# Optimization experiments

Measured on AMD Instinct MI355X. Metric: run time of the kernel, lower is better.

## Reference

```python
import jax, jax.numpy as jnp
import numpy as np

SAMPLE_RATE = 48000.0
WIN_SIZE = 512   # also the FFT size (nfft = win_size in forward)
HOP_SIZE = 256   # win_size // 2, COLA with Hann
B = 128
NUM_FREQ_PTS = 96000  # 2 s RIR at 48 kHz


def _hann(n):
    # torch.hann_window default is periodic: 0.5*(1 - cos(2*pi*k/n))
    k = jnp.arange(n, dtype=jnp.float32)
    return 0.5 * (1.0 - jnp.cos(2.0 * jnp.pi * k / n))


def _stft(x, win, nfft, hop):
    # x: [B, L] real. center=False, onesided=True, not normalized.
    L = x.shape[-1]
    pad = (-L) % hop  # pad to multiple of hop, as in get_stft_torch
    if pad:
        x = jnp.pad(x, ((0, 0), (0, pad)))
    T = (x.shape[-1] - nfft) // hop + 1  # number of frames
    idx = hop * jnp.arange(T)[:, None] + jnp.arange(nfft)[None, :]  # [T, nfft]
    frames = x[:, idx] * win  # [B, T, nfft]
    return jnp.fft.rfft(frames, n=nfft, axis=-1)  # [B, T, F], F = nfft//2 + 1


def _edr_db(S):
    # S: [B, T, F] complex. EDR[m] = sum_{t>=m} |S[t]|^2  -> reverse cumsum (O(T)).
    P = jnp.abs(S) ** 2  # [B, T, F]
    edr = jnp.flip(jnp.cumsum(jnp.flip(P, axis=1), axis=1), axis=1)
    return 10.0 * jnp.log10(edr)  # db(..., is_squared=True)


def reference(target_re, target_im, ach_re, ach_im):
    n = target_re.shape[-1]
    target_rir = jnp.fft.irfft(target_re + 1j * target_im, n=n)
    ach_rir = jnp.fft.irfft(ach_re + 1j * ach_im, n=n)
    win = _hann(WIN_SIZE)
    S_t = _stft(target_rir, win, WIN_SIZE, HOP_SIZE)
    S_a = _stft(ach_rir, win, WIN_SIZE, HOP_SIZE)
    edr_t = _edr_db(S_t)
    edr_a = _edr_db(S_a)
    return jnp.sum(jnp.abs(edr_t - edr_a)) / jnp.sum(jnp.abs(edr_t))


def setup_inputs() -> dict:
    key = jax.random.key(0)
    k1, k2, k3, k4 = jax.random.split(key, 4)
    shape = (B, NUM_FREQ_PTS)
    return {
        "target_re": jax.random.normal(k1, shape, dtype=jnp.float32),
        "target_im": jax.random.normal(k2, shape, dtype=jnp.float32),
        "ach_re": jax.random.normal(k3, shape, dtype=jnp.float32),
        "ach_im": jax.random.normal(k4, shape, dtype=jnp.float32),
    }
```

## Files before the change

### kernel.cpp

```cpp
#include <hip/hip_runtime.h>
#include <math.h>

#define BATCH   128
#define NFREQ   96000
#define M_HALF  48000
#define NFRAMES 374
#define NBINS   257
#define NG      11
#define GLEN    34
#define FPW     4

#define PI_D 3.14159265358979323846

__device__ __forceinline__ float2 cmulf(float2 a, float2 b) {
  return make_float2(a.x * b.x - a.y * b.y, a.x * b.y + a.y * b.x);
}

__device__ __forceinline__ void bfly4(float2 z0, float2 z1, float2 z2, float2 z3,
                                      float2& o0, float2& o1, float2& o2, float2& o3) {
  float2 e0 = make_float2(z0.x + z2.x, z0.y + z2.y);
  float2 e1 = make_float2(z0.x - z2.x, z0.y - z2.y);
  float2 e2 = make_float2(z1.x + z3.x, z1.y + z3.y);
  float2 e3 = make_float2(z1.x - z3.x, z1.y - z3.y);
  o0 = make_float2(e0.x + e2.x, e0.y + e2.y);
  o2 = make_float2(e0.x - e2.x, e0.y - e2.y);
  o1 = make_float2(e1.x + e3.y, e1.y - e3.x);
  o3 = make_float2(e1.x - e3.y, e1.y + e3.x);
}

#define PIDX(i) ((i) + ((i) >> 3))

__global__ void setup_kernel(float2* __restrict__ Wm, float2* __restrict__ Wpack,
                             float2* __restrict__ W512, float* __restrict__ hann) {
  int i = blockIdx.x * blockDim.x + threadIdx.x;
  if (i < M_HALF) {
    double th = 2.0 * PI_D * (double)i / (double)M_HALF;
    double s, c; sincos(th, &s, &c);
    Wm[i] = make_float2((float)c, (float)s);
    double th2 = PI_D * (double)i / (double)M_HALF;
    double s2, c2; sincos(th2, &s2, &c2);
    Wpack[i] = make_float2((float)c2, (float)s2);
  }
  if (i < 512) {
    double th = -2.0 * PI_D * (double)i / 512.0;
    double s, c; sincos(th, &s, &c);
    W512[i] = make_float2((float)c, (float)s);
    hann[i] = (float)(0.5 * (1.0 - cos(2.0 * PI_D * (double)i / 512.0)));
  }
}

__global__ __launch_bounds__(256) void pack_kernel(
    const float* __restrict__ tre, const float* __restrict__ tim,
    const float* __restrict__ are, const float* __restrict__ aim,
    float2* __restrict__ A, const float2* __restrict__ Wpack, int b0, int c) {
  int idx = blockIdx.x * blockDim.x + threadIdx.x;
  int total = 2 * c * M_HALF;
  if (idx >= total) return;
  int row = idx / M_HALF;
  int k = idx - row * M_HALF;
  int isA = row >= c;
  int b = b0 + (isA ? row - c : row);
  const float* re = isA ? are : tre;
  const float* im = isA ? aim : tim;
  const float* rr = re + (size_t)b * NFREQ;
  const float* ii = im + (size_t)b * NFREQ;
  float xr = rr[k];
  float xi = (k == 0) ? 0.f : ii[k];
  int mk = M_HALF - k;
  float yr = rr[mk];
  float yi = (mk == M_HALF) ? 0.f : ii[mk];
  float Er = 0.5f * (xr + yr);
  float Ei = 0.5f * (xi - yi);
  float Dr = 0.5f * (xr - yr);
  float Di = 0.5f * (xi + yi);
  float2 wp = Wpack[k];
  float tr = wp.x * Dr - wp.y * Di;
  float ti = wp.x * Di + wp.y * Dr;
  const float sc = 1.0f / (float)M_HALF;
  A[(size_t)row * M_HALF + k] = make_float2((Er - ti) * sc, (Ei + tr) * sc);
}

template <int R, int S, int NN>
__global__ __launch_bounds__(256) void stage_kernel(
    const float2* __restrict__ x, float2* __restrict__ y,
    const float2* __restrict__ Wm, int rows) {
  constexpr int MM = NN / R;
  constexpr int ITEMS = M_HALF / R;
  int idx = blockIdx.x * blockDim.x + threadIdx.x;
  if (idx >= rows * ITEMS) return;
  int row = idx / ITEMS;
  int t = idx - row * ITEMS;
  int q = t % S;
  int p = t / S;
  const float2* xr = x + (size_t)row * M_HALF;
  float2* yr = y + (size_t)row * M_HALF;
  float2 a[R];
#pragma unroll
  for (int j = 0; j < R; ++j) a[j] = xr[q + S * (p + MM * j)];
  float2 wr[R];
#pragma unroll
  for (int t2 = 0; t2 < R; ++t2) wr[t2] = Wm[t2 * (M_HALF / R)];
  float2 twb = Wm[(size_t)p * (M_HALF / NN)];
  float2 tw = make_float2(1.f, 0.f);
#pragma unroll
  for (int u = 0; u < R; ++u) {
    float2 acc = a[0];
#pragma unroll
    for (int j = 1; j < R; ++j) {
      float2 w = wr[(u * j) % R];
      acc.x += a[j].x * w.x - a[j].y * w.y;
      acc.y += a[j].x * w.y + a[j].y * w.x;
    }
    acc = cmulf(acc, tw);
    yr[q + S * (R * p + u)] = acc;
    tw = cmulf(tw, twb);
  }
}

__global__ __launch_bounds__(256) void stft256_kernel(
    const float* __restrict__ xtime, float* __restrict__ P,
    const float2* __restrict__ W512, const float* __restrict__ hann) {
  __shared__ float2 lds[4][2][288];
  const int tid = threadIdx.x;
  const int wave = tid >> 6;
  const int l = tid & 63;
  const int row = blockIdx.y;
  const int frame0 = (blockIdx.x * 4 + wave) * FPW;

  float2* Abuf = lds[wave][0];
  float2* Bbuf = lds[wave][1];

  const float2* hann2 = (const float2*)hann;
  float2 hw[4];
#pragma unroll
  for (int j = 0; j < 4; ++j) hw[j] = hann2[l + 64 * j];
  float2 t1[3], t2[3], t3[3];
  {
    int p2 = l >> 2, p3 = l >> 4;
#pragma unroll
    for (int u = 1; u <= 3; ++u) {
      t1[u - 1] = W512[2 * u * l];
      t2[u - 1] = W512[8 * u * p2];
      t3[u - 1] = W512[32 * u * p3];
    }
  }

  const float2* xrow = (const float2*)xtime + (size_t)row * 48000;

  for (int fi = 0; fi < FPW; ++fi) {
    const int fr = frame0 + fi;
    const bool active = (fr < NFRAMES);
    float2 z[4];
    if (active) {
      const float2* src = xrow + fr * 128;
#pragma unroll
      for (int j = 0; j < 4; ++j) {
        float2 v = src[l + 64 * j];
        z[j] = make_float2(v.x * hw[j].x, v.y * hw[j].y);
      }
    } else {
#pragma unroll
      for (int j = 0; j < 4; ++j) z[j] = make_float2(0.f, 0.f);
    }
    float2 o0, o1, o2, o3;
    bfly4(z[0], z[1], z[2], z[3], o0, o1, o2, o3);
    o1 = cmulf(o1, t1[0]); o2 = cmulf(o2, t1[1]); o3 = cmulf(o3, t1[2]);
    Abuf[PIDX(4 * l + 0)] = o0; Abuf[PIDX(4 * l + 1)] = o1;
    Abuf[PIDX(4 * l + 2)] = o2; Abuf[PIDX(4 * l + 3)] = o3;
    __syncthreads();
    {
      int q = l & 3, p = l >> 2;
      float2 a0 = Abuf[PIDX(q + 4 * p)];
      float2 a1 = Abuf[PIDX(q + 4 * (p + 16))];
      float2 a2 = Abuf[PIDX(q + 4 * (p + 32))];
      float2 a3 = Abuf[PIDX(q + 4 * (p + 48))];
      bfly4(a0, a1, a2, a3, o0, o1, o2, o3);
      o1 = cmulf(o1, t2[0]); o2 = cmulf(o2, t2[1]); o3 = cmulf(o3, t2[2]);
      int wb = q + 16 * p;
      Bbuf[PIDX(wb)] = o0; Bbuf[PIDX(wb + 4)] = o1;
      Bbuf[PIDX(wb + 8)] = o2; Bbuf[PIDX(wb + 12)] = o3;
    }
    __syncthreads();
    {
      int q = l & 15, p = l >> 4;
      float2 a0 = Bbuf[PIDX(q + 16 * p)];
      float2 a1 = Bbuf[PIDX(q + 16 * (p + 4))];
      float2 a2 = Bbuf[PIDX(q + 16 * (p + 8))];
      float2 a3 = Bbuf[PIDX(q + 16 * (p + 12))];
      bfly4(a0, a1, a2, a3, o0, o1, o2, o3);
      o1 = cmulf(o1, t3[0]); o2 = cmulf(o2, t3[1]); o3 = cmulf(o3, t3[2]);
      int wb = q + 64 * p;
      Abuf[PIDX(wb)] = o0; Abuf[PIDX(wb + 16)] = o1;
      Abuf[PIDX(wb + 32)] = o2; Abuf[PIDX(wb + 48)] = o3;
    }
    __syncthreads();
    {
      float2 a0 = Abuf[PIDX(l)];
      float2 a1 = Abuf[PIDX(l + 64)];
      float2 a2 = Abuf[PIDX(l + 128)];
      float2 a3 = Abuf[PIDX(l + 192)];
      bfly4(a0, a1, a2, a3, o0, o1, o2, o3);
      Bbuf[PIDX(l)] = o0; Bbuf[PIDX(l + 64)] = o1;
      Bbuf[PIDX(l + 128)] = o2; Bbuf[PIDX(l + 192)] = o3;
    }
    __syncthreads();
    if (active) {
      float* Prow = P + ((size_t)row * NFRAMES + fr) * NBINS;
      for (int k = l; k <= 256; k += 64) {
        float2 Zk = Bbuf[PIDX(k & 255)];
        float2 Zm = Bbuf[PIDX((256 - k) & 255)];
        float2 E  = make_float2(0.5f * (Zk.x + Zm.x), 0.5f * (Zk.y - Zm.y));
        float2 Op = make_float2(Zk.x - Zm.x, Zk.y + Zm.y);
        float2 Od = make_float2(0.5f * Op.y, -0.5f * Op.x);
        float2 W  = W512[k];
        float2 X  = make_float2(E.x + W.x * Od.x - W.y * Od.y,
                                E.y + W.x * Od.y + W.y * Od.x);
        Prow[k] = X.x * X.x + X.y * X.y;
      }
    }
    __syncthreads();
  }
}

__global__ __launch_bounds__(256) void edrA_kernel(const float* __restrict__ P,
                                                   float* __restrict__ part) {
  const int r = blockIdx.x;
  const int g = blockIdx.y;
  const float* Pr = P + (size_t)r * (NFRAMES * NBINS);
  for (int bin = threadIdx.x; bin < NBINS; bin += 256) {
    float s = 0.f;
    const int m0 = g * GLEN;
    for (int m = m0; m < m0 + GLEN; ++m) s += Pr[m * NBINS + bin];
    part[((size_t)r * NG + g) * NBINS + bin] = s;
  }
}

__global__ __launch_bounds__(256) void edrB_kernel(const float* __restrict__ P,
                                                   const float* __restrict__ part,
                                                   double* __restrict__ accum, int c) {
  const int b = blockIdx.x;
  const int g = blockIdx.y;
  const float* Pt = P + (size_t)b * (NFRAMES * NBINS);
  const float* Pa = P + (size_t)(b + c) * (NFRAMES * NBINS);
  const float* qt = part + (size_t)b * NG * NBINS;
  const float* qa = part + (size_t)(b + c) * NG * NBINS;
  float sn = 0.f, sd = 0.f;
  for (int bin = threadIdx.x; bin < NBINS; bin += 256) {
    float ct = 0.f, ca = 0.f;
    for (int g2 = g + 1; g2 < NG; ++g2) {
      ct += qt[g2 * NBINS + bin];
      ca += qa[g2 * NBINS + bin];
    }
    const int m0 = g * GLEN;
    for (int m = m0 + GLEN - 1; m >= m0; --m) {
      ct += Pt[m * NBINS + bin];
      ca += Pa[m * NBINS + bin];
      float lt = 10.f * log10f(ct);
      float la = 10.f * log10f(ca);
      sn += fabsf(lt - la);
      sd += fabsf(lt);
    }
  }
#pragma unroll
  for (int off = 32; off > 0; off >>= 1) {
    sn += __shfl_down(sn, off, 64);
    sd += __shfl_down(sd, off, 64);
  }
  __shared__ float wsn[4], wsd[4];
  const int wave = threadIdx.x >> 6;
  if ((threadIdx.x & 63) == 0) { wsn[wave] = sn; wsd[wave] = sd; }
  __syncthreads();
  if (threadIdx.x == 0) {
    float tn = 0.f, td = 0.f;
#pragma unroll
    for (int w = 0; w < 4; ++w) { tn += wsn[w]; td += wsd[w]; }
    int slot = (blockIdx.x * NG + blockIdx.y) & 63;
    atomicAdd(&accum[slot], (double)tn);
    atomicAdd(&accum[64 + slot], (double)td);
  }
}

__global__ void final_kernel(const double* __restrict__ accum, float* __restrict__ out) {
  double n = 0.0, d = 0.0;
  for (int i = 0; i < 64; ++i) { n += accum[i]; d += accum[64 + i]; }
  out[0] = (float)(n / d);
}

extern "C" void kernel_launch(void* const* d_in, const int* in_sizes, int n_in,
                              void* d_out, int out_size, void* d_ws, size_t ws_size,
                              hipStream_t stream) {
  const float* tre = (const float*)d_in[0];
  const float* tim = (const float*)d_in[1];
  const float* are = (const float*)d_in[2];
  const float* aim = (const float*)d_in[3];
  float* out = (float*)d_out;

  char* base = (char*)d_ws;
  size_t off = 0;
  auto take = [&](size_t bytes) -> char* {
    char* p = base + off;
    off += (bytes + 255) & ~(size_t)255;
    return p;
  };
  float2* Wm    = (float2*)take((size_t)M_HALF * sizeof(float2));
  float2* Wpack = (float2*)take((size_t)M_HALF * sizeof(float2));
  float2* W512  = (float2*)take(512 * sizeof(float2));
  float*  hann  = (float*)take(512 * sizeof(float));
  double* accum = (double*)take(128 * sizeof(double));
  size_t fixed = off;

  const size_t perA    = (size_t)2 * M_HALF * sizeof(float2);
  const size_t perP    = (size_t)2 * NFRAMES * NBINS * sizeof(float);
  const size_t perPart = (size_t)2 * NG * NBINS * sizeof(float);
  int c = 1;
  const int cands[8] = {128, 64, 32, 16, 8, 4, 2, 1};
  for (int ci = 0; ci < 8; ++ci) {
    size_t need = fixed + ((cands[ci] * perA + 255) & ~(size_t)255)
                        + ((cands[ci] * perP + 255) & ~(size_t)255)
                        + ((cands[ci] * perPart + 255) & ~(size_t)255);
    if (need <= ws_size) { c = cands[ci]; break; }
  }
  float2* A  = (float2*)take((size_t)c * perA);
  char*   BP = take((size_t)c * perP);
  float*  part = (float*)take((size_t)c * perPart);
  float2* Bb = (float2*)BP;
  float*  P  = (float*)BP;

  setup_kernel<<<(M_HALF + 255) / 256, 256, 0, stream>>>(Wm, Wpack, W512, hann);
  hipMemsetAsync(accum, 0, 128 * sizeof(double), stream);

  for (int b0 = 0; b0 < BATCH; b0 += c) {
    int rows = 2 * c;
    int tot = rows * M_HALF;
    pack_kernel<<<(tot + 255) / 256, 256, 0, stream>>>(tre, tim, are, aim, A, Wpack, b0, c);
    {
      int items = rows * (M_HALF / 15);
      stage_kernel<15, 1, 48000><<<(items + 255) / 256, 256, 0, stream>>>(A, Bb, Wm, rows);
    }
    {
      int items = rows * (M_HALF / 16);
      stage_kernel<16, 15, 3200><<<(items + 255) / 256, 256, 0, stream>>>(Bb, A, Wm, rows);
    }
    {
      int items = rows * (M_HALF / 10);
      stage_kernel<10, 240, 200><<<(items + 255) / 256, 256, 0, stream>>>(A, Bb, Wm, rows);
    }
    {
      int items = rows * (M_HALF / 20);
      stage_kernel<20, 2400, 20><<<(items + 255) / 256, 256, 0, stream>>>(Bb, A, Wm, rows);
    }
    {
      dim3 grid((NFRAMES + 4 * FPW - 1) / (4 * FPW), rows);
      stft256_kernel<<<grid, 256, 0, stream>>>((const float*)A, P, W512, hann);
    }
    edrA_kernel<<<dim3(rows, NG), 256, 0, stream>>>(P, part);
    edrB_kernel<<<dim3(c, NG), 256, 0, stream>>>(P, part, accum, c);
  }
  final_kernel<<<1, 1, 0, stream>>>(accum, out);
}
```

Measured before the change: 488.5 us.

## Replace five-pass global FFT with two LDS-resident four-step FFT kernels

The pack step and four global-memory radix stages of the 48000-point inverse FFT are replaced by a four-step 240x200 decomposition. Each part runs as one kernel doing its sub-FFT passes in shared memory with twiddles applied between, so full-row global round trips drop from five to two. The STFT kernel also swaps block-wide barriers for a per-wave LDS wait, since each wave owns its own buffers. The strided global writes and small grids (25 and 30 blocks per row) may limit coalescing and occupancy.

```diff
diff --git a/kernel.cpp b/kernel.cpp
--- a/kernel.cpp
+++ b/kernel.cpp
@@ -10,7 +10,12 @@
 #define GLEN    34
 #define FPW     4
 
+#define CS1 246
+#define CS2 206
+
 #define PI_D 3.14159265358979323846
+
+#define WAVE_SYNC() __asm__ volatile("s_waitcnt lgkmcnt(0)" ::: "memory")
 
 __device__ __forceinline__ float2 cmulf(float2 a, float2 b) {
   return make_float2(a.x * b.x - a.y * b.y, a.x * b.y + a.y * b.x);
@@ -28,10 +33,24 @@
   o3 = make_float2(e1.x - e3.y, e1.y + e3.x);
 }
 
+__device__ __forceinline__ void bfly4i(float2 z0, float2 z1, float2 z2, float2 z3,
+                                       float2& o0, float2& o1, float2& o2, float2& o3) {
+  float2 e0 = make_float2(z0.x + z2.x, z0.y + z2.y);
+  float2 e1 = make_float2(z0.x - z2.x, z0.y - z2.y);
+  float2 e2 = make_float2(z1.x + z3.x, z1.y + z3.y);
+  float2 e3 = make_float2(z1.x - z3.x, z1.y - z3.y);
+  o0 = make_float2(e0.x + e2.x, e0.y + e2.y);
+  o2 = make_float2(e0.x - e2.x, e0.y - e2.y);
+  o1 = make_float2(e1.x - e3.y, e1.y + e3.x);
+  o3 = make_float2(e1.x + e3.y, e1.y - e3.x);
+}
+
 #define PIDX(i) ((i) + ((i) >> 3))
 
 __global__ void setup_kernel(float2* __restrict__ Wm, float2* __restrict__ Wpack,
-                             float2* __restrict__ W512, float* __restrict__ hann) {
+                             float2* __restrict__ W512, float* __restrict__ hann,
+                             float2* __restrict__ W240, float2* __restrict__ W200,
+                             float2* __restrict__ Wp240) {
   int i = blockIdx.x * blockDim.x + threadIdx.x;
   if (i < M_HALF) {
     double th = 2.0 * PI_D * (double)i / (double)M_HALF;
@@ -47,73 +66,214 @@
     W512[i] = make_float2((float)c, (float)s);
     hann[i] = (float)(0.5 * (1.0 - cos(2.0 * PI_D * (double)i / 512.0)));
   }
-}
-
-__global__ __launch_bounds__(256) void pack_kernel(
+  if (i < 240) {
+    double th = 2.0 * PI_D * (double)i / 240.0;
+    double s, c; sincos(th, &s, &c);
+    W240[i] = make_float2((float)c, (float)s);
+    double th2 = PI_D * (double)i / 240.0;
+    double s2, c2; sincos(th2, &s2, &c2);
+    Wp240[i] = make_float2((float)c2, (float)s2);
+  }
+  if (i < 200) {
+    double th = 2.0 * PI_D * (double)i / 200.0;
+    double s, c; sincos(th, &s, &c);
+    W200[i] = make_float2((float)c, (float)s);
+  }
+}
+
+__global__ __launch_bounds__(256) void k1_kernel(
     const float* __restrict__ tre, const float* __restrict__ tim,
     const float* __restrict__ are, const float* __restrict__ aim,
-    float2* __restrict__ A, const float2* __restrict__ Wpack, int b0, int c) {
-  int idx = blockIdx.x * blockDim.x + threadIdx.x;
-  int total = 2 * c * M_HALF;
-  if (idx >= total) return;
-  int row = idx / M_HALF;
-  int k = idx - row * M_HALF;
-  int isA = row >= c;
-  int b = b0 + (isA ? row - c : row);
-  const float* re = isA ? are : tre;
-  const float* im = isA ? aim : tim;
-  const float* rr = re + (size_t)b * NFREQ;
-  const float* ii = im + (size_t)b * NFREQ;
-  float xr = rr[k];
-  float xi = (k == 0) ? 0.f : ii[k];
-  int mk = M_HALF - k;
-  float yr = rr[mk];
-  float yi = (mk == M_HALF) ? 0.f : ii[mk];
-  float Er = 0.5f * (xr + yr);
-  float Ei = 0.5f * (xi - yi);
-  float Dr = 0.5f * (xr - yr);
-  float Di = 0.5f * (xi + yi);
-  float2 wp = Wpack[k];
-  float tr = wp.x * Dr - wp.y * Di;
-  float ti = wp.x * Di + wp.y * Dr;
-  const float sc = 1.0f / (float)M_HALF;
-  A[(size_t)row * M_HALF + k] = make_float2((Er - ti) * sc, (Ei + tr) * sc);
-}
-
-template <int R, int S, int NN>
-__global__ __launch_bounds__(256) void stage_kernel(
-    const float2* __restrict__ x, float2* __restrict__ y,
-    const float2* __restrict__ Wm, int rows) {
-  constexpr int MM = NN / R;
-  constexpr int ITEMS = M_HALF / R;
-  int idx = blockIdx.x * blockDim.x + threadIdx.x;
-  if (idx >= rows * ITEMS) return;
-  int row = idx / ITEMS;
-  int t = idx - row * ITEMS;
-  int q = t % S;
-  int p = t / S;
-  const float2* xr = x + (size_t)row * M_HALF;
-  float2* yr = y + (size_t)row * M_HALF;
-  float2 a[R];
-#pragma unroll
-  for (int j = 0; j < R; ++j) a[j] = xr[q + S * (p + MM * j)];
-  float2 wr[R];
-#pragma unroll
-  for (int t2 = 0; t2 < R; ++t2) wr[t2] = Wm[t2 * (M_HALF / R)];
-  float2 twb = Wm[(size_t)p * (M_HALF / NN)];
-  float2 tw = make_float2(1.f, 0.f);
-#pragma unroll
-  for (int u = 0; u < R; ++u) {
-    float2 acc = a[0];
-#pragma unroll
-    for (int j = 1; j < R; ++j) {
-      float2 w = wr[(u * j) % R];
-      acc.x += a[j].x * w.x - a[j].y * w.y;
-      acc.y += a[j].x * w.y + a[j].y * w.x;
-    }
-    acc = cmulf(acc, tw);
-    yr[q + S * (R * p + u)] = acc;
-    tw = cmulf(tw, twb);
+    float2* __restrict__ G, const float2* __restrict__ Wm,
+    const float2* __restrict__ Wpack, const float2* __restrict__ Wp240,
+    const float2* __restrict__ W240, int b0, int c) {
+  __shared__ float2 LA[8 * CS1];
+  __shared__ float2 LB[8 * CS1];
+  const int tid = threadIdx.x;
+  const int row = blockIdx.y;
+  const int K0 = blockIdx.x * 8;
+
+  const int isA = row >= c;
+  const int b = b0 + (isA ? row - c : row);
+  const float* rr = (isA ? are : tre) + (size_t)b * NFREQ;
+  const float* ii = (isA ? aim : tim) + (size_t)b * NFREQ;
+
+  {
+    const int k1o = tid & 7;
+    const float2 wpa = Wpack[K0 + k1o];
+    const float sc = 1.0f / (float)M_HALF;
+    for (int e = tid; e < 8 * 240; e += 256) {
+      int k2 = e >> 3;
+      int k = K0 + k1o + 200 * k2;
+      float xr = rr[k];
+      float xi = (k == 0) ? 0.f : ii[k];
+      int mk = M_HALF - k;
+      float yr = rr[mk];
+      float yi = (k == 0) ? 0.f : ii[mk];
+      float Er = 0.5f * (xr + yr);
+      float Ei = 0.5f * (xi - yi);
+      float Dr = 0.5f * (xr - yr);
+      float Di = 0.5f * (xi + yi);
+      float2 wp = cmulf(wpa, Wp240[k2]);
+      float tr = wp.x * Dr - wp.y * Di;
+      float ti = wp.x * Di + wp.y * Dr;
+      LA[k1o * CS1 + k2] = make_float2((Er - ti) * sc, (Ei + tr) * sc);
+    }
+  }
+  __syncthreads();
+  for (int e = tid; e < 8 * 60; e += 256) {
+    int col = e & 7, p = e >> 3;
+    const float2* in = LA + col * CS1;
+    float2 o0, o1, o2, o3;
+    bfly4i(in[p], in[p + 60], in[p + 120], in[p + 180], o0, o1, o2, o3);
+    o1 = cmulf(o1, W240[p]);
+    o2 = cmulf(o2, W240[2 * p]);
+    o3 = cmulf(o3, W240[3 * p]);
+    float2* out = LB + col * CS1 + 4 * p;
+    out[0] = o0; out[1] = o1; out[2] = o2; out[3] = o3;
+  }
+  __syncthreads();
+  for (int e = tid; e < 8 * 60; e += 256) {
+    int col = e & 7, t = e >> 3;
+    int q = t & 3, p = t >> 2;
+    const float2* in = LB + col * CS1;
+    float2 o0, o1, o2, o3;
+    bfly4i(in[q + 4 * p], in[q + 4 * (p + 15)], in[q + 4 * (p + 30)],
+           in[q + 4 * (p + 45)], o0, o1, o2, o3);
+    o1 = cmulf(o1, W240[4 * p]);
+    o2 = cmulf(o2, W240[8 * p]);
+    o3 = cmulf(o3, W240[12 * p]);
+    float2* out = LA + col * CS1 + q;
+    out[4 * (4 * p + 0)] = o0; out[4 * (4 * p + 1)] = o1;
+    out[4 * (4 * p + 2)] = o2; out[4 * (4 * p + 3)] = o3;
+  }
+  __syncthreads();
+  {
+    float2 w15[15];
+#pragma unroll
+    for (int m = 0; m < 15; ++m) w15[m] = W240[16 * m];
+    for (int e = tid; e < 8 * 16; e += 256) {
+      int col = e & 7, q = e >> 3;
+      const float2* in = LA + col * CS1 + q;
+      float2 a[15];
+#pragma unroll
+      for (int j = 0; j < 15; ++j) a[j] = in[16 * j];
+      float2* out = LB + col * CS1 + q;
+#pragma unroll
+      for (int u = 0; u < 15; ++u) {
+        float2 acc = a[0];
+#pragma unroll
+        for (int j = 1; j < 15; ++j) {
+          float2 w = w15[(u * j) % 15];
+          acc.x += a[j].x * w.x - a[j].y * w.y;
+          acc.y += a[j].x * w.y + a[j].y * w.x;
+        }
+        out[16 * u] = acc;
+      }
+    }
+  }
+  __syncthreads();
+  {
+    const int col = tid & 7;
+    const int k1 = K0 + col;
+    int n2 = tid >> 3;
+    float2 tw = Wm[k1 * n2];
+    const float2 twstep = Wm[32 * k1];
+    float2* Grow = G + (size_t)row * M_HALF;
+    const float2* in = LB + col * CS1;
+    for (; n2 < 240; n2 += 32) {
+      Grow[(size_t)n2 * 200 + k1] = cmulf(in[n2], tw);
+      tw = cmulf(tw, twstep);
+    }
+  }
+}
+
+__global__ __launch_bounds__(256) void k2_kernel(
+    const float2* __restrict__ G, float2* __restrict__ X,
+    const float2* __restrict__ W200) {
+  __shared__ float2 LA[8 * CS2];
+  __shared__ float2 LB[8 * CS2];
+  const int tid = threadIdx.x;
+  const int row = blockIdx.y;
+  const int N20 = blockIdx.x * 8;
+  const float2* Grow = G + (size_t)row * M_HALF;
+
+  for (int e = tid; e < 8 * 200; e += 256) {
+    int n2o = e / 200;
+    int k1 = e - n2o * 200;
+    LA[n2o * CS2 + k1] = Grow[(size_t)(N20 + n2o) * 200 + k1];
+  }
+  __syncthreads();
+  for (int e = tid; e < 8 * 50; e += 256) {
+    int col = e & 7, p = e >> 3;
+    const float2* in = LA + col * CS2;
+    float2 o0, o1, o2, o3;
+    bfly4i(in[p], in[p + 50], in[p + 100], in[p + 150], o0, o1, o2, o3);
+    o1 = cmulf(o1, W200[p]);
+    o2 = cmulf(o2, W200[2 * p]);
+    o3 = cmulf(o3, W200[3 * p]);
+    float2* out = LB + col * CS2 + 4 * p;
+    out[0] = o0; out[1] = o1; out[2] = o2; out[3] = o3;
+  }
+  __syncthreads();
+  {
+    float2 w5[5];
+#pragma unroll
+    for (int m = 0; m < 5; ++m) w5[m] = W200[40 * m];
+    for (int e = tid; e < 8 * 40; e += 256) {
+      int col = e & 7, t = e >> 3;
+      int q = t & 3, p = t >> 2;
+      const float2* in = LB + col * CS2 + q;
+      float2 a[5];
+#pragma unroll
+      for (int j = 0; j < 5; ++j) a[j] = in[4 * (p + 10 * j)];
+      float2* out = LA + col * CS2 + q;
+#pragma unroll
+      for (int u = 0; u < 5; ++u) {
+        float2 acc = a[0];
+#pragma unroll
+        for (int j = 1; j < 5; ++j) {
+          float2 w = w5[(u * j) % 5];
+          acc.x += a[j].x * w.x - a[j].y * w.y;
+          acc.y += a[j].x * w.y + a[j].y * w.x;
+        }
+        acc = cmulf(acc, W200[4 * u * p]);
+        out[4 * (5 * p + u)] = acc;
+      }
+    }
+  }
+  __syncthreads();
+  {
+    float2 w10[10];
+#pragma unroll
+    for (int m = 0; m < 10; ++m) w10[m] = W200[20 * m];
+    for (int e = tid; e < 8 * 20; e += 256) {
+      int col = e & 7, q = e >> 3;
+      const float2* in = LA + col * CS2 + q;
+      float2 a[10];
+#pragma unroll
+      for (int j = 0; j < 10; ++j) a[j] = in[20 * j];
+      float2* out = LB + col * CS2 + q;
+#pragma unroll
+      for (int u = 0; u < 10; ++u) {
+        float2 acc = a[0];
+#pragma unroll
+        for (int j = 1; j < 10; ++j) {
+          float2 w = w10[(u * j) % 10];
+          acc.x += a[j].x * w.x - a[j].y * w.y;
+          acc.y += a[j].x * w.y + a[j].y * w.x;
+        }
+        out[20 * u] = acc;
+      }
+    }
+  }
+  __syncthreads();
+  {
+    const int n2o = tid & 7;
+    float2* Xrow = X + (size_t)row * M_HALF + (N20 + n2o);
+    const float2* in = LB + n2o * CS2;
+    for (int n1 = tid >> 3; n1 < 200; n1 += 32)
+      Xrow[240 * n1] = in[n1];
   }
 }
 
@@ -167,7 +327,7 @@
     o1 = cmulf(o1, t1[0]); o2 = cmulf(o2, t1[1]); o3 = cmulf(o3, t1[2]);
     Abuf[PIDX(4 * l + 0)] = o0; Abuf[PIDX(4 * l + 1)] = o1;
     Abuf[PIDX(4 * l + 2)] = o2; Abuf[PIDX(4 * l + 3)] = o3;
-    __syncthreads();
+    WAVE_SYNC();
     {
       int q = l & 3, p = l >> 2;
       float2 a0 = Abuf[PIDX(q + 4 * p)];
@@ -180,7 +340,7 @@
       Bbuf[PIDX(wb)] = o0; Bbuf[PIDX(wb + 4)] = o1;
       Bbuf[PIDX(wb + 8)] = o2; Bbuf[PIDX(wb + 12)] = o3;
     }
-    __syncthreads();
+    WAVE_SYNC();
     {
       int q = l & 15, p = l >> 4;
       float2 a0 = Bbuf[PIDX(q + 16 * p)];
@@ -193,7 +353,7 @@
       Abuf[PIDX(wb)] = o0; Abuf[PIDX(wb + 16)] = o1;
       Abuf[PIDX(wb + 32)] = o2; Abuf[PIDX(wb + 48)] = o3;
     }
-    __syncthreads();
+    WAVE_SYNC();
     {
       float2 a0 = Abuf[PIDX(l)];
       float2 a1 = Abuf[PIDX(l + 64)];
@@ -203,7 +363,7 @@
       Bbuf[PIDX(l)] = o0; Bbuf[PIDX(l + 64)] = o1;
       Bbuf[PIDX(l + 128)] = o2; Bbuf[PIDX(l + 192)] = o3;
     }
-    __syncthreads();
+    WAVE_SYNC();
     if (active) {
       float* Prow = P + ((size_t)row * NFRAMES + fr) * NBINS;
       for (int k = l; k <= 256; k += 64) {
@@ -213,12 +373,12 @@
         float2 Op = make_float2(Zk.x - Zm.x, Zk.y + Zm.y);
         float2 Od = make_float2(0.5f * Op.y, -0.5f * Op.x);
         float2 W  = W512[k];
-        float2 X  = make_float2(E.x + W.x * Od.x - W.y * Od.y,
+        float2 Xb = make_float2(E.x + W.x * Od.x - W.y * Od.y,
                                 E.y + W.x * Od.y + W.y * Od.x);
-        Prow[k] = X.x * X.x + X.y * X.y;
+        Prow[k] = Xb.x * Xb.x + Xb.y * Xb.y;
       }
     }
-    __syncthreads();
+    WAVE_SYNC();
   }
 }
 
@@ -306,6 +466,9 @@
   float2* Wpack = (float2*)take((size_t)M_HALF * sizeof(float2));
   float2* W512  = (float2*)take(512 * sizeof(float2));
   float*  hann  = (float*)take(512 * sizeof(float));
+  float2* W240  = (float2*)take(240 * sizeof(float2));
+  float2* W200  = (float2*)take(200 * sizeof(float2));
+  float2* Wp240 = (float2*)take(240 * sizeof(float2));
   double* accum = (double*)take(128 * sizeof(double));
   size_t fixed = off;
 
@@ -320,38 +483,24 @@
                         + ((cands[ci] * perPart + 255) & ~(size_t)255);
     if (need <= ws_size) { c = cands[ci]; break; }
   }
-  float2* A  = (float2*)take((size_t)c * perA);
-  char*   BP = take((size_t)c * perP);
+  float2* Z    = (float2*)take((size_t)c * perA);
+  char*   BP   = take((size_t)c * perP);
   float*  part = (float*)take((size_t)c * perPart);
-  float2* Bb = (float2*)BP;
-  float*  P  = (float*)BP;
-
-  setup_kernel<<<(M_HALF + 255) / 256, 256, 0, stream>>>(Wm, Wpack, W512, hann);
+  float2* G = (float2*)BP;
+  float*  P = (float*)BP;
+
+  setup_kernel<<<(M_HALF + 255) / 256, 256, 0, stream>>>(Wm, Wpack, W512, hann,
+                                                         W240, W200, Wp240);
   hipMemsetAsync(accum, 0, 128 * sizeof(double), stream);
 
   for (int b0 = 0; b0 < BATCH; b0 += c) {
     int rows = 2 * c;
-    int tot = rows * M_HALF;
-    pack_kernel<<<(tot + 255) / 256, 256, 0, stream>>>(tre, tim, are, aim, A, Wpack, b0, c);
-    {
-      int items = rows * (M_HALF / 15);
-      stage_kernel<15, 1, 48000><<<(items + 255) / 256, 256, 0, stream>>>(A, Bb, Wm, rows);
-    }
-    {
-      int items = rows * (M_HALF / 16);
-      stage_kernel<16, 15, 3200><<<(items + 255) / 256, 256, 0, stream>>>(Bb, A, Wm, rows);
-    }
-    {
-      int items = rows * (M_HALF / 10);
-      stage_kernel<10, 240, 200><<<(items + 255) / 256, 256, 0, stream>>>(A, Bb, Wm, rows);
-    }
-    {
-      int items = rows * (M_HALF / 20);
-      stage_kernel<20, 2400, 20><<<(items + 255) / 256, 256, 0, stream>>>(Bb, A, Wm, rows);
-    }
+    k1_kernel<<<dim3(25, rows), 256, 0, stream>>>(tre, tim, are, aim, G, Wm,
+                                                  Wpack, Wp240, W240, b0, c);
+    k2_kernel<<<dim3(30, rows), 256, 0, stream>>>(G, Z, W200);
     {
       dim3 grid((NFRAMES + 4 * FPW - 1) / (4 * FPW), rows);
-      stft256_kernel<<<grid, 256, 0, stream>>>((const float*)A, P, W512, hann);
+      stft256_kernel<<<grid, 256, 0, stream>>>((const float*)Z, P, W512, hann);
     }
     edrA_kernel<<<dim3(rows, NG), 256, 0, stream>>>(P, part);
     edrB_kernel<<<dim3(c, NG), 256, 0, stream>>>(P, part, accum, c);
```

Result: faster. 451.9 us (-7.5%).
